# Performance work log

Hardware: AMD Instinct MI355X
Metric: run time of the kernel (lower is better)

## Reference

```python
import jax, jax.numpy as jnp
import numpy as np
import math

S, B, D = 2048, 2, 1024
H = 16
DH = D // H
WIN = 256
DIL = 1


def setup_inputs() -> dict:
    key = jax.random.key(0)
    ks = jax.random.split(key, 10)
    std = 1.0 / math.sqrt(D)
    return {
        "x": jax.random.normal(ks[0], (S, B, D), jnp.float32),
        "beta": jax.random.normal(ks[1], (H,), jnp.float32) * 0.02,
        "Wq": jax.random.normal(ks[2], (D, D), jnp.float32) * std,
        "bq": jnp.zeros((D,), jnp.float32),
        "Wk": jax.random.normal(ks[3], (D, D), jnp.float32) * std,
        "bk": jnp.zeros((D,), jnp.float32),
        "Wv": jax.random.normal(ks[4], (D, D), jnp.float32) * std,
        "bv": jnp.zeros((D,), jnp.float32),
        "Wo": jax.random.normal(ks[5], (D, D), jnp.float32) * std,
        "bo": jnp.zeros((D,), jnp.float32),
    }


def _split_heads(t):
    # (S, B, D) -> (B*H, S, DH), matching rearrange 's b (h d) -> (b h) s d'
    return t.reshape(S, B, H, DH).transpose(1, 2, 0, 3).reshape(B * H, S, DH)


def reference(x, beta, Wq, bq, Wk, bk, Wv, bv, Wo, bo):
    q = _split_heads(x @ Wq + bq)
    k = _split_heads(x @ Wk + bk)
    v = _split_heads(x @ Wv + bv)

    # per-head learnable temperature: q / (sqrt(d_head) * exp(beta))
    beta_exp = jnp.tile(jnp.exp(beta), B)  # (B*H,), head index = z % H
    q = q / (jnp.sqrt(jnp.asarray(DH, x.dtype)) * beta_exp)[:, None, None]

    # causal dilated windowed mask
    idx = jnp.arange(S)
    diff = idx[:, None] - idx[None, :]
    allowed = (diff >= 0) & (diff <= DIL * (WIN - 1)) & (diff % DIL == 0)
    mask = jnp.where(allowed, jnp.asarray(0.0, x.dtype), jnp.asarray(-jnp.inf, x.dtype))

    scores = jnp.einsum('zqd,zkd->zqk', q, k) + mask[None]
    # attention sink: extra zero-logit column absorbing probability mass
    scores = jnp.concatenate([scores, jnp.zeros((B * H, S, 1), scores.dtype)], axis=-1)
    attn = jax.nn.softmax(scores, axis=-1)[..., :-1]

    out = jnp.einsum('zqk,zkd->zqd', attn, v)
    # (B*H, S, DH) -> (S, B, D)
    out = out.reshape(B, H, S, DH).transpose(2, 0, 1, 3).reshape(S, B, D)
    return out @ Wo + bo
```

## Files before the change

### kernel.cpp

```cpp
#include <hip/hip_runtime.h>
#include <math.h>

#define S_LEN  2048
#define BATCH  2
#define DM     1024
#define NHEAD  16
#define DHEAD  64
#define WIN    256
#define MROWS  4096

#define PPAD 68

#define BM 128
#define BN 192
#define BK 64
#define NKT (DM / BK)

#define OM 128
#define ON 64

typedef __attribute__((ext_vector_type(8))) short bf16x8;
typedef __attribute__((ext_vector_type(4))) float f32x4;

__device__ __forceinline__ unsigned short f2b(float f) {
    unsigned int u = __float_as_uint(f);
    return (unsigned short)((u + 0x7fffu + ((u >> 16) & 1u)) >> 16);
}
__device__ __forceinline__ void gld16(const void* g, void* l) {
    __builtin_amdgcn_global_load_lds(
        (const __attribute__((address_space(1))) void*)g,
        (__attribute__((address_space(3))) void*)l, 16, 0, 0);
}
__device__ __forceinline__ bf16x8 pack8(float4 a, float4 b) {
    bf16x8 r;
    r[0] = (short)f2b(a.x); r[1] = (short)f2b(a.y);
    r[2] = (short)f2b(a.z); r[3] = (short)f2b(a.w);
    r[4] = (short)f2b(b.x); r[5] = (short)f2b(b.y);
    r[6] = (short)f2b(b.z); r[7] = (short)f2b(b.w);
    return r;
}

__global__ __launch_bounds__(256)
void cvtx(const float* __restrict__ x, unsigned short* __restrict__ xb)
{
    const int i = (blockIdx.x * 256 + threadIdx.x) * 4;
    float4 f = *(const float4*)(x + i);
    ushort4 o; o.x = f2b(f.x); o.y = f2b(f.y); o.z = f2b(f.z); o.w = f2b(f.w);
    *(ushort4*)(xb + i) = o;
}

__global__ __launch_bounds__(256)
void twcvt4(const float* __restrict__ W0, const float* __restrict__ W1,
            const float* __restrict__ W2, const float* __restrict__ W3,
            unsigned short* __restrict__ T0, unsigned short* __restrict__ T1,
            unsigned short* __restrict__ T2, unsigned short* __restrict__ T3)
{
    const int zz = blockIdx.z;
    const float* W = (zz == 0) ? W0 : (zz == 1) ? W1 : (zz == 2) ? W2 : W3;
    unsigned short* WT = (zz == 0) ? T0 : (zz == 1) ? T1 : (zz == 2) ? T2 : T3;

    __shared__ float t32[32][33];
    const int bx = blockIdx.x * 32;
    const int by = blockIdx.y * 32;
    const int c  = threadIdx.x & 31;
    const int r0 = threadIdx.x >> 5;
#pragma unroll
    for (int p = 0; p < 4; ++p)
        t32[r0 + 8 * p][c] = W[(size_t)(by + r0 + 8 * p) * DM + bx + c];
    __syncthreads();
#pragma unroll
    for (int p = 0; p < 4; ++p)
        WT[(size_t)(bx + r0 + 8 * p) * DM + by + c] = f2b(t32[c][r0 + 8 * p]);
}

__global__ __launch_bounds__(256, 2)
void gemm_qkv(const unsigned short* __restrict__ A,
              const unsigned short* __restrict__ BT,
              const float* __restrict__ b0,
              const float* __restrict__ b1,
              const float* __restrict__ b2,
              const float* __restrict__ beta,
              unsigned short* __restrict__ Cb)
{
    __shared__ unsigned short Ab[2][BM * BK];
    __shared__ unsigned short Bb[2][BN * BK];

    const int t   = threadIdx.x;
    const int ln  = t & 63;
    const int wv  = t >> 6;
    const int wr  = wv & 1;
    const int wc  = wv >> 1;
    const int m16 = ln & 15;
    const int g   = ln >> 4;
    const int sw  = m16 & 7;

    const int rowBase = blockIdx.y * BM;
    const int colBase = blockIdx.x * BN;

    const int sr  = t >> 3;
    const int scx = (t & 7) ^ (sr & 7);
    const size_t gOff = (size_t)sr * DM + scx * 8;
    const int    ldOff = t * 8;

    f32x4 acc[4][6];
#pragma unroll
    for (int u = 0; u < 4; ++u)
#pragma unroll
        for (int v = 0; v < 6; ++v)
            acc[u][v] = (f32x4){0.f, 0.f, 0.f, 0.f};

    const unsigned short* aBase = A  + (size_t)rowBase * DM + gOff;
    const unsigned short* bBase = BT + (size_t)colBase * DM + gOff;

    {
#pragma unroll
        for (int ca = 0; ca < 2; ++ca)
#pragma unroll
            for (int hf = 0; hf < 2; ++hf)
                gld16(aBase + (size_t)(ca * 64 + hf * 32) * DM,
                      &Ab[0][ca * 4096 + hf * 2048 + ldOff]);
#pragma unroll
        for (int cb = 0; cb < 3; ++cb)
#pragma unroll
            for (int hf = 0; hf < 2; ++hf)
                gld16(bBase + (size_t)(cb * 64 + hf * 32) * DM,
                      &Bb[0][cb * 4096 + hf * 2048 + ldOff]);
        asm volatile("s_waitcnt vmcnt(0)" ::: "memory");
        __builtin_amdgcn_s_barrier();
        __builtin_amdgcn_sched_barrier(0);
    }

    for (int kt = 0; kt < NKT; ++kt) {
        const int cur = kt & 1;
        const unsigned short* Ac = Ab[cur];
        const unsigned short* Bc = Bb[cur];
        unsigned short* An = Ab[cur ^ 1];
        unsigned short* Bn = Bb[cur ^ 1];
        const bool hn = (kt < NKT - 1);
        const unsigned short* aS = aBase + (size_t)(kt + 1) * BK;
        const unsigned short* bS = bBase + (size_t)(kt + 1) * BK;

        bf16x8 af0[4], bf0[6];
#pragma unroll
        for (int u = 0; u < 4; ++u)
            af0[u] = *(const bf16x8*)&Ac[(wr * 64 + u * 16 + m16) * BK + ((g ^ sw) * 8)];
#pragma unroll
        for (int v = 0; v < 6; ++v)
            bf0[v] = *(const bf16x8*)&Bc[(wc * 96 + v * 16 + m16) * BK + ((g ^ sw) * 8)];

        if (hn) {
#pragma unroll
            for (int ca = 0; ca < 2; ++ca)
#pragma unroll
                for (int hf = 0; hf < 2; ++hf)
                    gld16(aS + (size_t)(ca * 64 + hf * 32) * DM,
                          &An[ca * 4096 + hf * 2048 + ldOff]);
#pragma unroll
            for (int cb = 0; cb < 3; ++cb)
#pragma unroll
                for (int hf = 0; hf < 2; ++hf)
                    gld16(bS + (size_t)(cb * 64 + hf * 32) * DM,
                          &Bn[cb * 4096 + hf * 2048 + ldOff]);
        }

        __builtin_amdgcn_s_setprio(1);
#pragma unroll
        for (int u = 0; u < 4; ++u)
#pragma unroll
            for (int v = 0; v < 6; ++v)
                acc[u][v] = __builtin_amdgcn_mfma_f32_16x16x32_bf16(
                    af0[u], bf0[v], acc[u][v], 0, 0, 0);
        __builtin_amdgcn_s_setprio(0);

        bf16x8 af1[4], bf1[6];
#pragma unroll
        for (int u = 0; u < 4; ++u)
            af1[u] = *(const bf16x8*)&Ac[(wr * 64 + u * 16 + m16) * BK + (((4 | g) ^ sw) * 8)];
#pragma unroll
        for (int v = 0; v < 6; ++v)
            bf1[v] = *(const bf16x8*)&Bc[(wc * 96 + v * 16 + m16) * BK + (((4 | g) ^ sw) * 8)];

        __builtin_amdgcn_s_setprio(1);
#pragma unroll
        for (int u = 0; u < 4; ++u)
#pragma unroll
            for (int v = 0; v < 6; ++v)
                acc[u][v] = __builtin_amdgcn_mfma_f32_16x16x32_bf16(
                    af1[u], bf1[v], acc[u][v], 0, 0, 0);
        __builtin_amdgcn_s_setprio(0);

        if (hn)
            asm volatile("s_waitcnt vmcnt(0)" ::: "memory");
        __builtin_amdgcn_s_barrier();
        __builtin_amdgcn_sched_barrier(0);
    }

    const int q4 = g * 4;
#pragma unroll
    for (int v = 0; v < 6; ++v) {
        const int col = colBase + wc * 96 + v * 16 + m16;
        const int sec = col >> 10;
        const int h   = (col >> 6) & (NHEAD - 1);
        const int dh  = col & 63;
        if (sec < 2) {
            const float bi = (sec == 0 ? b0 : b1)[col & (DM - 1)];
            const float sc = (sec == 0) ? 0.125f * __expf(-beta[h]) : 1.0f;
            unsigned short* base = Cb + (size_t)sec * MROWS * DM;
#pragma unroll
            for (int u = 0; u < 4; ++u)
#pragma unroll
                for (int r = 0; r < 4; ++r) {
                    const int row = rowBase + wr * 64 + u * 16 + q4 + r;
                    const int s = row >> 1, bb = row & 1;
                    const int z = bb * NHEAD + h;
                    base[((size_t)z * S_LEN + s) * DHEAD + dh] =
                        f2b((acc[u][v][r] + bi) * sc);
                }
        } else {
            unsigned short* vtb = Cb + (size_t)2 * MROWS * DM;
            const float bi = b2[col & (DM - 1)];
#pragma unroll
            for (int u = 0; u < 4; ++u) {
                const int row0 = rowBase + wr * 64 + u * 16 + q4;
                const int s0   = row0 >> 1;
                ushort2 p0, p1;
                p0.x = f2b(acc[u][v][0] + bi);
                p0.y = f2b(acc[u][v][2] + bi);
                p1.x = f2b(acc[u][v][1] + bi);
                p1.y = f2b(acc[u][v][3] + bi);
                *(ushort2*)(vtb + ((size_t)(h * DHEAD + dh) * S_LEN + s0)) = p0;
                *(ushort2*)(vtb + ((size_t)((NHEAD + h) * DHEAD + dh) * S_LEN + s0)) = p1;
            }
        }
    }
}

__global__ __launch_bounds__(256, 2)
void gemm_out(const unsigned short* __restrict__ A,
              const unsigned short* __restrict__ BT,
              const float* __restrict__ bias,
              float* __restrict__ Cf)
{
    __shared__ unsigned short As[2][OM * BK];
    __shared__ unsigned short Bs[2][ON * BK];

    const int t  = threadIdx.x;
    const int wv = t >> 6, ln = t & 63;
    const int wr = wv >> 1, wc = wv & 1;
    const int m16 = ln & 15, g = ln >> 4;
    const int sw  = m16 & 7;

    const int rowBase = blockIdx.y * OM;
    const int colBase = blockIdx.x * ON;

    const int sr  = t >> 3;
    const int scx = (t & 7) ^ (sr & 7);
    const size_t gOff = (size_t)sr * DM + scx * 8;
    const int    ldOff = t * 8;

    f32x4 acc[4][2];
#pragma unroll
    for (int u = 0; u < 4; ++u)
#pragma unroll
        for (int v = 0; v < 2; ++v)
            acc[u][v] = (f32x4){0.f, 0.f, 0.f, 0.f};

    {
        const unsigned short* a0 = A  + (size_t)rowBase * DM + gOff;
        const unsigned short* bt = BT + (size_t)colBase * DM + gOff;
#pragma unroll
        for (int j = 0; j < 4; ++j)
            gld16(a0 + (size_t)(j * 32) * DM, &As[0][j * 2048 + ldOff]);
#pragma unroll
        for (int j = 0; j < 2; ++j)
            gld16(bt + (size_t)(j * 32) * DM, &Bs[0][j * 2048 + ldOff]);
        asm volatile("s_waitcnt vmcnt(0)" ::: "memory");
        __builtin_amdgcn_s_barrier();
        __builtin_amdgcn_sched_barrier(0);
    }

    for (int kt = 0; kt < DM / BK; ++kt) {
        const int cur = kt & 1;
        const unsigned short* Ac = As[cur];
        const unsigned short* Bc = Bs[cur];
        unsigned short* An = As[cur ^ 1];
        unsigned short* Bn = Bs[cur ^ 1];
        const bool hn = (kt < DM / BK - 1);
        const unsigned short* aS = A  + (size_t)rowBase * DM + (kt + 1) * BK + gOff;
        const unsigned short* bS = BT + (size_t)colBase * DM + (kt + 1) * BK + gOff;

        bf16x8 af0[4], bf0[2];
#pragma unroll
        for (int u = 0; u < 4; ++u)
            af0[u] = *(const bf16x8*)&Ac[(wr * 64 + u * 16 + m16) * BK + ((g ^ sw) * 8)];
#pragma unroll
        for (int v = 0; v < 2; ++v)
            bf0[v] = *(const bf16x8*)&Bc[(wc * 32 + v * 16 + m16) * BK + ((g ^ sw) * 8)];

        if (hn) {
#pragma unroll
            for (int j = 0; j < 4; ++j)
                gld16(aS + (size_t)(j * 32) * DM, &An[j * 2048 + ldOff]);
#pragma unroll
            for (int j = 0; j < 2; ++j)
                gld16(bS + (size_t)(j * 32) * DM, &Bn[j * 2048 + ldOff]);
        }

        __builtin_amdgcn_s_setprio(1);
#pragma unroll
        for (int u = 0; u < 4; ++u)
#pragma unroll
            for (int v = 0; v < 2; ++v)
                acc[u][v] = __builtin_amdgcn_mfma_f32_16x16x32_bf16(
                    af0[u], bf0[v], acc[u][v], 0, 0, 0);
        __builtin_amdgcn_s_setprio(0);

        bf16x8 af1[4], bf1[2];
#pragma unroll
        for (int u = 0; u < 4; ++u)
            af1[u] = *(const bf16x8*)&As[cur][(wr * 64 + u * 16 + m16) * BK + (((4 | g) ^ sw) * 8)];
#pragma unroll
        for (int v = 0; v < 2; ++v)
            bf1[v] = *(const bf16x8*)&Bs[cur][(wc * 32 + v * 16 + m16) * BK + (((4 | g) ^ sw) * 8)];

        __builtin_amdgcn_s_setprio(1);
#pragma unroll
        for (int u = 0; u < 4; ++u)
#pragma unroll
            for (int v = 0; v < 2; ++v)
                acc[u][v] = __builtin_amdgcn_mfma_f32_16x16x32_bf16(
                    af1[u], bf1[v], acc[u][v], 0, 0, 0);
        __builtin_amdgcn_s_setprio(0);

        if (hn)
            asm volatile("s_waitcnt vmcnt(0)" ::: "memory");
        __builtin_amdgcn_s_barrier();
        __builtin_amdgcn_sched_barrier(0);
    }

    const int q4 = g * 4;
#pragma unroll
    for (int v = 0; v < 2; ++v) {
        const int col = colBase + wc * 32 + v * 16 + m16;
        const float bi = bias[col];
#pragma unroll
        for (int u = 0; u < 4; ++u)
#pragma unroll
            for (int r = 0; r < 4; ++r) {
                const int row = rowBase + wr * 64 + u * 16 + q4 + r;
                Cf[(size_t)row * DM + col] = acc[u][v][r] + bi;
            }
    }
}

__global__ __launch_bounds__(256, 3)
void attn_mfma(const unsigned short* __restrict__ q,
               const unsigned short* __restrict__ k,
               const unsigned short* __restrict__ vt,
               unsigned short* __restrict__ ao)
{
    __shared__ unsigned short Ks[2][64 * 64];
    __shared__ unsigned short Vs[2][64 * 64];
    __shared__ float Ps[64][PPAD];

    const int t   = threadIdx.x;
    const int wv  = t >> 6, ln = t & 63;
    const int m16 = ln & 15, g = ln >> 4;
    const int sw  = m16 & 7;
    const int z   = blockIdx.y;
    const int q0  = blockIdx.x * 64;
    const size_t zbase = (size_t)z * S_LEN * DHEAD;

    const int sr  = t >> 3;
    const int scx = (t & 7) ^ (sr & 7);
    const unsigned short* kS = k  + zbase + (size_t)sr * DHEAD + scx * 8;
    const unsigned short* vS = vt + ((size_t)z * DHEAD + sr) * S_LEN + scx * 8;
    const int ldOff = t * 8;

    const unsigned short* qrow = q + zbase + (size_t)(q0 + wv * 16 + m16) * DHEAD;
    bf16x8 qf0 = *(const bf16x8*)(qrow + g * 8);
    bf16x8 qf1 = *(const bf16x8*)(qrow + 32 + g * 8);

    f32x4 oacc[4];
#pragma unroll
    for (int v4 = 0; v4 < 4; ++v4) oacc[v4] = (f32x4){0.f, 0.f, 0.f, 0.f};
    float lr[4];
#pragma unroll
    for (int r = 0; r < 4; ++r) lr[r] = 1.f;

    const int c0 = (blockIdx.x < 4) ? (4 - (int)blockIdx.x) : 0;

    {
        const int kb = q0 - 256 + c0 * 64;
        gld16(kS + (size_t)kb * DHEAD,        &Ks[0][ldOff]);
        gld16(kS + (size_t)(kb + 32) * DHEAD, &Ks[0][2048 + ldOff]);
        gld16(vS + kb,                        &Vs[0][ldOff]);
        gld16(vS + (size_t)32 * S_LEN + kb,   &Vs[0][2048 + ldOff]);
        asm volatile("s_waitcnt vmcnt(0)" ::: "memory");
        __builtin_amdgcn_s_barrier();
        __builtin_amdgcn_sched_barrier(0);
    }

    for (int c = c0; c < 5; ++c) {
        const int cur = (c - c0) & 1;
        const int kb  = q0 - 256 + c * 64;
        const bool hn = (c < 4);

        if (hn) {
            const int kn = kb + 64;
            gld16(kS + (size_t)kn * DHEAD,        &Ks[cur ^ 1][ldOff]);
            gld16(kS + (size_t)(kn + 32) * DHEAD, &Ks[cur ^ 1][2048 + ldOff]);
            gld16(vS + kn,                        &Vs[cur ^ 1][ldOff]);
            gld16(vS + (size_t)32 * S_LEN + kn,   &Vs[cur ^ 1][2048 + ldOff]);
        }

        f32x4 sacc[4];
#pragma unroll
        for (int v4 = 0; v4 < 4; ++v4) {
            sacc[v4] = (f32x4){0.f, 0.f, 0.f, 0.f};
            bf16x8 kf0 = *(const bf16x8*)&Ks[cur][(v4 * 16 + m16) * 64 + ((g ^ sw) * 8)];
            sacc[v4] = __builtin_amdgcn_mfma_f32_16x16x32_bf16(qf0, kf0, sacc[v4], 0, 0, 0);
            bf16x8 kf1 = *(const bf16x8*)&Ks[cur][(v4 * 16 + m16) * 64 + (((4 | g) ^ sw) * 8)];
            sacc[v4] = __builtin_amdgcn_mfma_f32_16x16x32_bf16(qf1, kf1, sacc[v4], 0, 0, 0);
        }

        const bool mhi = (c == 4), mlo = (c == 0);
#pragma unroll
        for (int r = 0; r < 4; ++r) {
            const int ig = q0 + wv * 16 + g * 4 + r;
            float rsum = 0.f;
#pragma unroll
            for (int v4 = 0; v4 < 4; ++v4) {
                const int jg = kb + v4 * 16 + m16;
                float x = sacc[v4][r];
                const bool valid = (!mhi || jg <= ig) && (!mlo || jg >= ig - (WIN - 1));
                x = valid ? x : -1e30f;
                const float pp = __expf(x);
                Ps[wv * 16 + g * 4 + r][v4 * 16 + m16] = pp;
                rsum += pp;
            }
#pragma unroll
            for (int off = 1; off < 16; off <<= 1)
                rsum += __shfl_xor(rsum, off, 64);
            lr[r] += rsum;
        }

        asm volatile("s_waitcnt lgkmcnt(0)" ::: "memory");
        __builtin_amdgcn_sched_barrier(0);

        const float* prow = &Ps[wv * 16 + m16][0];
        bf16x8 pf0 = pack8(*(const float4*)(prow + g * 8),
                           *(const float4*)(prow + g * 8 + 4));
        bf16x8 pf1 = pack8(*(const float4*)(prow + 32 + g * 8),
                           *(const float4*)(prow + 32 + g * 8 + 4));
#pragma unroll
        for (int v4 = 0; v4 < 4; ++v4) {
            bf16x8 vf0 = *(const bf16x8*)&Vs[cur][(v4 * 16 + m16) * 64 + ((g ^ sw) * 8)];
            oacc[v4] = __builtin_amdgcn_mfma_f32_16x16x32_bf16(pf0, vf0, oacc[v4], 0, 0, 0);
            bf16x8 vf1 = *(const bf16x8*)&Vs[cur][(v4 * 16 + m16) * 64 + (((4 | g) ^ sw) * 8)];
            oacc[v4] = __builtin_amdgcn_mfma_f32_16x16x32_bf16(pf1, vf1, oacc[v4], 0, 0, 0);
        }

        if (hn) {
            asm volatile("s_waitcnt vmcnt(0)" ::: "memory");
            __builtin_amdgcn_s_barrier();
            __builtin_amdgcn_sched_barrier(0);
        }
    }

    const int bb = z >> 4, h = z & 15;
#pragma unroll
    for (int r = 0; r < 4; ++r) {
        const int ig  = q0 + wv * 16 + g * 4 + r;
        const float inv = 1.f / lr[r];
#pragma unroll
        for (int v4 = 0; v4 < 4; ++v4)
            ao[(size_t)(ig * BATCH + bb) * DM + h * DHEAD + v4 * 16 + m16] =
                f2b(oacc[v4][r] * inv);
    }
}

extern "C" void kernel_launch(void* const* d_in, const int* in_sizes, int n_in,
                              void* d_out, int out_size, void* d_ws, size_t ws_size,
                              hipStream_t stream)
{
    const float* x    = (const float*)d_in[0];
    const float* beta = (const float*)d_in[1];
    const float* Wq   = (const float*)d_in[2];
    const float* bq   = (const float*)d_in[3];
    const float* Wk   = (const float*)d_in[4];
    const float* bk   = (const float*)d_in[5];
    const float* Wv   = (const float*)d_in[6];
    const float* bv   = (const float*)d_in[7];
    const float* Wo   = (const float*)d_in[8];
    const float* bo   = (const float*)d_in[9];
    float* out = (float*)d_out;

    unsigned short* w = (unsigned short*)d_ws;
    const size_t seg = (size_t)MROWS * DM;
    unsigned short* qb  = w;
    unsigned short* kb  = w + seg;
    unsigned short* vtb = w + 2 * seg;
    unsigned short* ab  = w + 3 * seg;
    unsigned short* xb  = w + 4 * seg;
    unsigned short* wtq = w + 5 * seg;
    unsigned short* wtk = wtq + (size_t)DM * DM;
    unsigned short* wtv = wtk + (size_t)DM * DM;
    unsigned short* wto = wtv + (size_t)DM * DM;

    cvtx<<<4096, 256, 0, stream>>>(x, xb);
    twcvt4<<<dim3(32, 32, 4), 256, 0, stream>>>(Wq, Wk, Wv, Wo, wtq, wtk, wtv, wto);

    gemm_qkv<<<dim3(3072 / BN, MROWS / BM), 256, 0, stream>>>(
        xb, wtq, bq, bk, bv, beta, qb);

    attn_mfma<<<dim3(S_LEN / 64, BATCH * NHEAD), 256, 0, stream>>>(qb, kb, vtb, ab);

    gemm_out<<<dim3(DM / ON, MROWS / OM), 256, 0, stream>>>(ab, wto, bo, out);
}
```

Baseline: 172.3 us.

## Shrink QKV GEMM tiles for higher occupancy and fuse x conversion into weight kernel

```diff
diff --git a/kernel.cpp b/kernel.cpp
--- a/kernel.cpp
+++ b/kernel.cpp
@@ -12,8 +12,8 @@
 #define PPAD 68
 
 #define BM 128
-#define BN 192
-#define BK 64
+#define BN 96
+#define BK 32
 #define NKT (DM / BK)
 
 #define OM 128
@@ -41,21 +41,27 @@
 }
 
 __global__ __launch_bounds__(256)
-void cvtx(const float* __restrict__ x, unsigned short* __restrict__ xb)
-{
-    const int i = (blockIdx.x * 256 + threadIdx.x) * 4;
-    float4 f = *(const float4*)(x + i);
-    ushort4 o; o.x = f2b(f.x); o.y = f2b(f.y); o.z = f2b(f.z); o.w = f2b(f.w);
-    *(ushort4*)(xb + i) = o;
-}
-
-__global__ __launch_bounds__(256)
 void twcvt4(const float* __restrict__ W0, const float* __restrict__ W1,
             const float* __restrict__ W2, const float* __restrict__ W3,
+            const float* __restrict__ x,
             unsigned short* __restrict__ T0, unsigned short* __restrict__ T1,
-            unsigned short* __restrict__ T2, unsigned short* __restrict__ T3)
+            unsigned short* __restrict__ T2, unsigned short* __restrict__ T3,
+            unsigned short* __restrict__ xb)
 {
     const int zz = blockIdx.z;
+    if (zz == 4) {
+        const int flat = blockIdx.y * 32 + blockIdx.x;
+        const int base = flat * 4096 + threadIdx.x * 4;
+#pragma unroll
+        for (int p = 0; p < 4; ++p) {
+            const int i = base + p * 1024;
+            float4 f = *(const float4*)(x + i);
+            ushort4 o;
+            o.x = f2b(f.x); o.y = f2b(f.y); o.z = f2b(f.z); o.w = f2b(f.w);
+            *(ushort4*)(xb + i) = o;
+        }
+        return;
+    }
     const float* W = (zz == 0) ? W0 : (zz == 1) ? W1 : (zz == 2) ? W2 : W3;
     unsigned short* WT = (zz == 0) ? T0 : (zz == 1) ? T1 : (zz == 2) ? T2 : T3;
 
@@ -73,7 +79,7 @@
         WT[(size_t)(bx + r0 + 8 * p) * DM + by + c] = f2b(t32[c][r0 + 8 * p]);
 }
 
-__global__ __launch_bounds__(256, 2)
+__global__ __launch_bounds__(256, 4)
 void gemm_qkv(const unsigned short* __restrict__ A,
               const unsigned short* __restrict__ BT,
               const float* __restrict__ b0,
@@ -88,43 +94,36 @@
     const int t   = threadIdx.x;
     const int ln  = t & 63;
     const int wv  = t >> 6;
-    const int wr  = wv & 1;
-    const int wc  = wv >> 1;
+    const int wr  = wv >> 1;
+    const int wc  = wv & 1;
     const int m16 = ln & 15;
     const int g   = ln >> 4;
-    const int sw  = m16 & 7;
+    const int swz = (m16 >> 1) & 3;
 
     const int rowBase = blockIdx.y * BM;
     const int colBase = blockIdx.x * BN;
 
-    const int sr  = t >> 3;
-    const int scx = (t & 7) ^ (sr & 7);
+    const int sr  = t >> 2;
+    const int scx = (t & 3) ^ ((sr >> 1) & 3);
     const size_t gOff = (size_t)sr * DM + scx * 8;
     const int    ldOff = t * 8;
 
-    f32x4 acc[4][6];
+    f32x4 acc[4][3];
 #pragma unroll
     for (int u = 0; u < 4; ++u)
 #pragma unroll
-        for (int v = 0; v < 6; ++v)
+        for (int v = 0; v < 3; ++v)
             acc[u][v] = (f32x4){0.f, 0.f, 0.f, 0.f};
 
     const unsigned short* aBase = A  + (size_t)rowBase * DM + gOff;
     const unsigned short* bBase = BT + (size_t)colBase * DM + gOff;
 
     {
-#pragma unroll
-        for (int ca = 0; ca < 2; ++ca)
-#pragma unroll
-            for (int hf = 0; hf < 2; ++hf)
-                gld16(aBase + (size_t)(ca * 64 + hf * 32) * DM,
-                      &Ab[0][ca * 4096 + hf * 2048 + ldOff]);
-#pragma unroll
-        for (int cb = 0; cb < 3; ++cb)
-#pragma unroll
-            for (int hf = 0; hf < 2; ++hf)
-                gld16(bBase + (size_t)(cb * 64 + hf * 32) * DM,
-                      &Bb[0][cb * 4096 + hf * 2048 + ldOff]);
+        gld16(aBase,                    &Ab[0][ldOff]);
+        gld16(aBase + (size_t)64 * DM,  &Ab[0][2048 + ldOff]);
+        gld16(bBase,                    &Bb[0][ldOff]);
+        if (t < 128)
+            gld16(bBase + (size_t)64 * DM, &Bb[0][2048 + ldOff]);
         asm volatile("s_waitcnt vmcnt(0)" ::: "memory");
         __builtin_amdgcn_s_barrier();
         __builtin_amdgcn_sched_barrier(0);
@@ -140,53 +139,29 @@
         const unsigned short* aS = aBase + (size_t)(kt + 1) * BK;
         const unsigned short* bS = bBase + (size_t)(kt + 1) * BK;
 
-        bf16x8 af0[4], bf0[6];
-#pragma unroll
-        for (int u = 0; u < 4; ++u)
-            af0[u] = *(const bf16x8*)&Ac[(wr * 64 + u * 16 + m16) * BK + ((g ^ sw) * 8)];
-#pragma unroll
-        for (int v = 0; v < 6; ++v)
-            bf0[v] = *(const bf16x8*)&Bc[(wc * 96 + v * 16 + m16) * BK + ((g ^ sw) * 8)];
-
         if (hn) {
-#pragma unroll
-            for (int ca = 0; ca < 2; ++ca)
-#pragma unroll
-                for (int hf = 0; hf < 2; ++hf)
-                    gld16(aS + (size_t)(ca * 64 + hf * 32) * DM,
-                          &An[ca * 4096 + hf * 2048 + ldOff]);
-#pragma unroll
-            for (int cb = 0; cb < 3; ++cb)
-#pragma unroll
-                for (int hf = 0; hf < 2; ++hf)
-                    gld16(bS + (size_t)(cb * 64 + hf * 32) * DM,
-                          &Bn[cb * 4096 + hf * 2048 + ldOff]);
-        }
+            gld16(aS,                   &An[ldOff]);
+            gld16(aS + (size_t)64 * DM, &An[2048 + ldOff]);
+            gld16(bS,                   &Bn[ldOff]);
+            if (t < 128)
+                gld16(bS + (size_t)64 * DM, &Bn[2048 + ldOff]);
+        }
+
+        bf16x8 af[4], bf[3];
+#pragma unroll
+        for (int u = 0; u < 4; ++u)
+            af[u] = *(const bf16x8*)&Ac[(wr * 64 + u * 16 + m16) * BK + ((g ^ swz) * 8)];
+#pragma unroll
+        for (int v = 0; v < 3; ++v)
+            bf[v] = *(const bf16x8*)&Bc[(wc * 48 + v * 16 + m16) * BK + ((g ^ swz) * 8)];
 
         __builtin_amdgcn_s_setprio(1);
 #pragma unroll
         for (int u = 0; u < 4; ++u)
 #pragma unroll
-            for (int v = 0; v < 6; ++v)
+            for (int v = 0; v < 3; ++v)
                 acc[u][v] = __builtin_amdgcn_mfma_f32_16x16x32_bf16(
-                    af0[u], bf0[v], acc[u][v], 0, 0, 0);
-        __builtin_amdgcn_s_setprio(0);
-
-        bf16x8 af1[4], bf1[6];
-#pragma unroll
-        for (int u = 0; u < 4; ++u)
-            af1[u] = *(const bf16x8*)&Ac[(wr * 64 + u * 16 + m16) * BK + (((4 | g) ^ sw) * 8)];
-#pragma unroll
-        for (int v = 0; v < 6; ++v)
-            bf1[v] = *(const bf16x8*)&Bc[(wc * 96 + v * 16 + m16) * BK + (((4 | g) ^ sw) * 8)];
-
-        __builtin_amdgcn_s_setprio(1);
-#pragma unroll
-        for (int u = 0; u < 4; ++u)
-#pragma unroll
-            for (int v = 0; v < 6; ++v)
-                acc[u][v] = __builtin_amdgcn_mfma_f32_16x16x32_bf16(
-                    af1[u], bf1[v], acc[u][v], 0, 0, 0);
+                    af[u], bf[v], acc[u][v], 0, 0, 0);
         __builtin_amdgcn_s_setprio(0);
 
         if (hn)
@@ -197,8 +172,8 @@
 
     const int q4 = g * 4;
 #pragma unroll
-    for (int v = 0; v < 6; ++v) {
-        const int col = colBase + wc * 96 + v * 16 + m16;
+    for (int v = 0; v < 3; ++v) {
+        const int col = colBase + wc * 48 + v * 16 + m16;
         const int sec = col >> 10;
         const int h   = (col >> 6) & (NHEAD - 1);
         const int dh  = col & 63;
@@ -241,8 +216,8 @@
               const float* __restrict__ bias,
               float* __restrict__ Cf)
 {
-    __shared__ unsigned short As[2][OM * BK];
-    __shared__ unsigned short Bs[2][ON * BK];
+    __shared__ unsigned short As[2][OM * 64];
+    __shared__ unsigned short Bs[2][ON * 64];
 
     const int t  = threadIdx.x;
     const int wv = t >> 6, ln = t & 63;
@@ -279,23 +254,23 @@
         __builtin_amdgcn_sched_barrier(0);
     }
 
-    for (int kt = 0; kt < DM / BK; ++kt) {
+    for (int kt = 0; kt < DM / 64; ++kt) {
         const int cur = kt & 1;
         const unsigned short* Ac = As[cur];
         const unsigned short* Bc = Bs[cur];
         unsigned short* An = As[cur ^ 1];
         unsigned short* Bn = Bs[cur ^ 1];
-        const bool hn = (kt < DM / BK - 1);
-        const unsigned short* aS = A  + (size_t)rowBase * DM + (kt + 1) * BK + gOff;
-        const unsigned short* bS = BT + (size_t)colBase * DM + (kt + 1) * BK + gOff;
+        const bool hn = (kt < DM / 64 - 1);
+        const unsigned short* aS = A  + (size_t)rowBase * DM + (kt + 1) * 64 + gOff;
+        const unsigned short* bS = BT + (size_t)colBase * DM + (kt + 1) * 64 + gOff;
 
         bf16x8 af0[4], bf0[2];
 #pragma unroll
         for (int u = 0; u < 4; ++u)
-            af0[u] = *(const bf16x8*)&Ac[(wr * 64 + u * 16 + m16) * BK + ((g ^ sw) * 8)];
+            af0[u] = *(const bf16x8*)&Ac[(wr * 64 + u * 16 + m16) * 64 + ((g ^ sw) * 8)];
 #pragma unroll
         for (int v = 0; v < 2; ++v)
-            bf0[v] = *(const bf16x8*)&Bc[(wc * 32 + v * 16 + m16) * BK + ((g ^ sw) * 8)];
+            bf0[v] = *(const bf16x8*)&Bc[(wc * 32 + v * 16 + m16) * 64 + ((g ^ sw) * 8)];
 
         if (hn) {
 #pragma unroll
@@ -318,10 +293,10 @@
         bf16x8 af1[4], bf1[2];
 #pragma unroll
         for (int u = 0; u < 4; ++u)
-            af1[u] = *(const bf16x8*)&As[cur][(wr * 64 + u * 16 + m16) * BK + (((4 | g) ^ sw) * 8)];
+            af1[u] = *(const bf16x8*)&Ac[(wr * 64 + u * 16 + m16) * 64 + (((4 | g) ^ sw) * 8)];
 #pragma unroll
         for (int v = 0; v < 2; ++v)
-            bf1[v] = *(const bf16x8*)&Bs[cur][(wc * 32 + v * 16 + m16) * BK + (((4 | g) ^ sw) * 8)];
+            bf1[v] = *(const bf16x8*)&Bc[(wc * 32 + v * 16 + m16) * 64 + (((4 | g) ^ sw) * 8)];
 
         __builtin_amdgcn_s_setprio(1);
 #pragma unroll
@@ -508,8 +483,8 @@
     unsigned short* wtv = wtk + (size_t)DM * DM;
     unsigned short* wto = wtv + (size_t)DM * DM;
 
-    cvtx<<<4096, 256, 0, stream>>>(x, xb);
-    twcvt4<<<dim3(32, 32, 4), 256, 0, stream>>>(Wq, Wk, Wv, Wo, wtq, wtk, wtv, wto);
+    twcvt4<<<dim3(32, 32, 5), 256, 0, stream>>>(
+        Wq, Wk, Wv, Wo, x, wtq, wtk, wtv, wto, xb);
 
     gemm_qkv<<<dim3(3072 / BN, MROWS / BM), 256, 0, stream>>>(
         xb, wtq, bq, bk, bv, beta, qb);
```

Result: no change. 175.7 us (+2.0%).
